# Kernel optimization log

Hardware: AMD Instinct MI355X
Metric: run time of the kernel (lower is better)

## Reference

```python
import jax, jax.numpy as jnp
import numpy as np

B, T, N, P, L = 8, 96, 20000, 12, 3
D = 32          # d_model (forced by channel-count identity d_model+96 == 4*d_model)
C = 4 * D       # 128 channels inside the linearized conv layers
M = 64          # random_feature_dim
TAU = 0.25
EPS = 1e-6      # numerical_stabilizer in random_feature_map


def _proj_matrix(m, d, seed=0):
    # create_random_matrix: stacked transposed-Q blocks from QR of gaussian blocks,
    # scaled row-wise by norms of a gaussian matrix (scaling=0).
    rng = np.random.RandomState(seed)
    blocks = []
    n_full = m // d
    for _ in range(n_full):
        q, _ = np.linalg.qr(rng.randn(d, d))
        blocks.append(q.T)
    rem = m - n_full * d
    if rem:
        q, _ = np.linalg.qr(rng.randn(d, d))
        blocks.append(q.T[:rem])
    mat = np.vstack(blocks)
    mult = np.linalg.norm(rng.randn(m, d), axis=1)
    return jnp.asarray(mult[:, None] * mat, dtype=jnp.float32)


def setup_inputs() -> dict:
    key = jax.random.key(0)
    ks = jax.random.split(key, 12)
    g = lambda k, shape, s=0.05: jax.random.normal(k, shape, jnp.float32) * s
    return {
        "x": jax.random.normal(ks[0], (B, T, N), jnp.float32),
        "x_mark": jax.random.uniform(ks[1], (B, T, 2), dtype=jnp.float32),
        "node_emb": g(ks[2], (N, D), 0.1),
        "time_tab": g(ks[3], (T, D), 0.1),
        "week_tab": g(ks[4], (7, D), 0.1),
        "input_w": g(ks[5], (D, 3 * T)),
        "input_b": jnp.zeros((D,), jnp.float32),
        "w1_w": g(ks[6], (D, 3 * D)),
        "w1_b": jnp.zeros((D,), jnp.float32),
        "w2_w": g(ks[7], (D, 3 * D)),
        "w2_b": jnp.zeros((D,), jnp.float32),
        "in_w": g(ks[8], (L, C, C)),
        "in_b": jnp.zeros((L, C), jnp.float32),
        "out_w": g(ks[9], (L, C, C)),
        "out_b": jnp.zeros((L, C), jnp.float32),
        "ln_g": jnp.ones((L, C), jnp.float32),
        "ln_b": jnp.zeros((L, C), jnp.float32),
        "reg_w": g(ks[10], (P, 2 * C)),
        "reg_b": jnp.zeros((P,), jnp.float32),
        "proj": _proj_matrix(M, D, seed=0),
    }


def _rfm(data, proj, is_query):
    # FAVOR+ positive random features (head dim == 1 folded out; shapes are [B,N,d])
    d = data.shape[-1]
    data = data * (float(d) ** -0.25)            # h(x) normalizer d^{-1/4}
    ratio = 1.0 / np.sqrt(float(proj.shape[0]))
    dash = jnp.einsum('bnd,md->bnm', data, proj)
    diag = 0.5 * jnp.sum(data * data, axis=-1, keepdims=True)
    if is_query:
        stab = jnp.max(dash, axis=-1, keepdims=True)          # per-row max
    else:
        stab = jnp.max(dash, axis=(1, 2), keepdims=True)      # max over features AND nodes
    return ratio * (jnp.exp(dash - diag - stab) + EPS)


def _linear_kernel(v, phi_q, phi_k):
    # associativity trick: (phi_q (phi_k^T v)) / (phi_q (phi_k^T 1))
    kv = jnp.einsum('bnm,bnc->bmc', phi_k, v)
    num = jnp.einsum('bnm,bmc->bnc', phi_q, kv)
    den = jnp.einsum('bnm,bm->bn', phi_q, jnp.sum(phi_k, axis=1))
    return num / den[..., None]


def reference(x, x_mark, node_emb, time_tab, week_tab, input_w, input_b,
              w1_w, w1_b, w2_w, w2_b, in_w, in_b, out_w, out_b,
              ln_g, ln_b, reg_w, reg_b, proj):
    Bq, Tq, Nq = x.shape
    marks = jax.lax.stop_gradient(x_mark)
    tod_idx = jnp.clip((marks[:, -1, 0] * Tq).astype(jnp.int32), 0, Tq - 1)
    dow_idx = jnp.clip((marks[:, -1, 1] * 7.0).astype(jnp.int32), 0, 6)
    time_e = jnp.broadcast_to(time_tab[tod_idx][:, None, :], (Bq, Nq, D))
    week_e = jnp.broadcast_to(week_tab[dow_idx][:, None, :], (Bq, Nq, D))
    node_e = jnp.broadcast_to(node_emb[None], (Bq, Nq, D))

    # input embedding over the flattened (feature-major) [3*T] channel axis
    tod_f = jnp.broadcast_to(x_mark[:, :, 0:1], (Bq, Tq, Nq))
    dow_f = jnp.broadcast_to(x_mark[:, :, 1:2], (Bq, Tq, Nq))
    feat = jnp.concatenate([x, tod_f, dow_f], axis=1)          # (B, 3T, N)
    x_in = jnp.einsum('bkn,ck->bnc', feat, input_w) + input_b  # (B, N, D)

    xg = jnp.concatenate([node_e, time_e, week_e], axis=-1)        # (B,N,3D)
    h = jnp.concatenate([x_in, node_e, time_e, week_e], axis=-1)   # (B,N,4D)

    inv_sqrt_tau = 1.0 / np.sqrt(TAU)
    nv1 = (jnp.einsum('bng,cg->bnc', xg, w1_w) + w1_b) * inv_sqrt_tau
    nv2 = (jnp.einsum('bng,cg->bnc', xg, w2_w) + w2_b) * inv_sqrt_tau
    # same node vectors (hence same data-derived seed / projection) every layer
    phi_q = _rfm(nv1, proj, True)    # (B,N,M)
    phi_k = _rfm(nv2, proj, False)   # (B,N,M)

    skip = h
    for i in range(L):
        res = h
        u = jax.nn.sigmoid(h @ in_w[i].T + in_b[i]) * (h @ out_w[i].T + out_b[i])
        u = _linear_kernel(u, phi_q, phi_k)
        h = u + res
        mu = jnp.mean(h, axis=-1, keepdims=True)
        var = jnp.var(h, axis=-1, keepdims=True)
        h = (h - mu) * jax.lax.rsqrt(var + 1e-5) * ln_g[i] + ln_b[i]

    out = jnp.concatenate([skip, h], axis=-1) @ reg_w.T + reg_b  # (B,N,P)
    return jnp.swapaxes(out, 1, 2)                               # (B,P,N)
```

## Files before the change

kernel.cpp:

```cpp
#include <hip/hip_runtime.h>

typedef unsigned short u16;
typedef __attribute__((ext_vector_type(8))) __bf16 bf16x8;
typedef __attribute__((ext_vector_type(4))) float f32x4;

#define BB 8
#define TT 96
#define NN 20000
#define NP 20160
#define PP 12
#define LL 3
#define DD 32
#define CC 128
#define MM 64
#define NB3 105
#define NB5 313
#define NB1 313

constexpr float KSC  = 0.8408964152537145f;
constexpr float KSC2 = 0.7071067811865476f;

__device__ inline u16 f2bf(float f){
  unsigned u = __float_as_uint(f);
  u = (u + 0x7fffu + ((u >> 16) & 1u)) >> 16;
  return (u16)u;
}
__device__ inline float bf2f(u16 h){ return __uint_as_float(((unsigned)h) << 16); }
__device__ inline unsigned fmapu(float f){
  unsigned u = __float_as_uint(f);
  return (u & 0x80000000u) ? ~u : (u | 0x80000000u);
}
__device__ inline float funmap(unsigned u){
  return (u & 0x80000000u) ? __uint_as_float(u & 0x7fffffffu) : __uint_as_float(~u);
}
__device__ inline unsigned pk2(float a, float b){
  return (unsigned)f2bf(a) | ((unsigned)f2bf(b) << 16);
}

__global__ void k0_prep(const float* xm, const float* time_tab, const float* week_tab,
                        const float* w1w, const float* w1b, const float* w2w, const float* w2b,
                        const float* inw, const float* inb, const float* proj,
                        float* bv1, float* bv2, float* sbd1, float* sbd2,
                        float* bc1, float* bc2, float* mb, int* tod, int* dow,
                        unsigned* cmx, float* ksum, float* qmat, float* emat)
{
  __shared__ float sT[BB][DD], sWk[BB][DD];
  __shared__ float sB1[BB][DD], sB2[BB][DD];
  __shared__ float sW1G[DD][DD], sW2G[DD][DD], sPJ[MM][DD];
  __shared__ int sTod[BB], sDow[BB];
  int tid = threadIdx.x;
  ksum[tid] = 0.f;
  for (int i = tid; i < DD*DD; i += 512){
    int c = i >> 5, g = i & 31;
    sW1G[c][g] = w1w[c*96 + g];
    sW2G[c][g] = w2w[c*96 + g];
  }
  for (int i = tid; i < MM*DD; i += 512) sPJ[i >> 5][i & 31] = proj[i];
  if (tid < BB){
    float t0 = xm[(tid*TT + TT-1)*2 + 0];
    float t1 = xm[(tid*TT + TT-1)*2 + 1];
    int ti = (int)(t0 * (float)TT); ti = min(max(ti, 0), TT-1);
    int di = (int)(t1 * 7.0f);      di = min(max(di, 0), 6);
    sTod[tid] = ti; sDow[tid] = di; tod[tid] = ti; dow[tid] = di;
  }
  if (tid < MM) cmx[tid] = fmapu(-3e38f);
  __syncthreads();
  if (tid < BB*DD){
    int b = tid >> 5, g = tid & 31;
    sT[b][g]  = time_tab[sTod[b]*DD + g];
    sWk[b][g] = week_tab[sDow[b]*DD + g];
  }
  __syncthreads();
  {
    int which = tid >> 8, b = (tid >> 5) & 7, c = tid & 31;
    const float* w  = which ? w2w : w1w;
    const float* wb = which ? w2b : w1b;
    float s = wb[c];
    for (int g = 0; g < DD; g++)
      s += sT[b][g]*w[c*96 + 32 + g] + sWk[b][g]*w[c*96 + 64 + g];
    if (which){ bv2[b*DD+c] = s; sB2[b][c] = s; }
    else      { bv1[b*DD+c] = s; sB1[b][c] = s; }
  }
  __syncthreads();
  for (int e = tid; e < 2*DD*MM; e += 512){
    int set = e >> 11, g = (e >> 6) & 31, m = e & 63;
    float s = 0.f;
    if (set == 0){ for (int c = 0; c < DD; c++) s += sW1G[c][g]*sPJ[m][c]; }
    else         { for (int c = 0; c < DD; c++) s += sW2G[c][g]*sPJ[m][c]; }
    qmat[e] = KSC * s;
  }
  {
    int set = tid >> 8, g = (tid >> 3) & 31, b = tid & 7;
    float s = 0.f;
    if (set == 0){ for (int c = 0; c < DD; c++) s += sW1G[c][g]*sB1[b][c]; }
    else         { for (int c = 0; c < DD; c++) s += sW2G[c][g]*sB2[b][c]; }
    emat[tid] = KSC2 * s;
  }
  {
    int b = tid >> 6, m = tid & 63;
    float s1 = 0.f, s2 = 0.f;
    for (int c = 0; c < DD; c++){
      float p = sPJ[m][c];
      s1 += sB1[b][c]*p; s2 += sB2[b][c]*p;
    }
    sbd1[b*MM+m] = KSC * s1;
    sbd2[b*MM+m] = KSC * s2;
  }
  if (tid < 16){
    int b = tid & 7;
    float s = 0.f;
    if (tid >> 3){ for (int c = 0; c < DD; c++) s += sB2[b][c]*sB2[b][c]; bc2[b] = 0.5f*KSC2*s; }
    else         { for (int c = 0; c < DD; c++) s += sB1[b][c]*sB1[b][c]; bc1[b] = 0.5f*KSC2*s; }
  }
  if (tid < 256){
    int b = tid >> 5, c = tid & 31;
    float s = inb[c];
    for (int t = 0; t < TT; t++){
      float m0 = xm[(b*TT+t)*2+0], m1 = xm[(b*TT+t)*2+1];
      s += m0 * inw[c*288 + 96 + t] + m1 * inw[c*288 + 192 + t];
    }
    mb[b*DD+c] = s;
  }
}

__global__ __launch_bounds__(256) void k1_node(
    const float* node_emb, const float* w1w, const float* w2w,
    const float* qmat, const float* emat,
    const float* gin_w, const float* gout_w,
    float* sd1, float* sd2, float* sq1, float* sq2,
    float* cr1, float* cr2, unsigned* cmx,
    u16* wbf, float* kvz)
{
  __shared__ float sQ1[DD*MM], sQ2[DD*MM];
  __shared__ float sW1[DD*DD], sW2[DD*DD];
  __shared__ float sE[2*DD*BB];
  __shared__ unsigned sCM[MM];
  int tid = threadIdx.x;
  int gid = blockIdx.x*256 + tid;
  const int TOT = NB1*256;
  for (int i = gid; i < LL*BB*MM*CC; i += TOT) kvz[i] = 0.f;
  for (int i = gid; i < 2*LL*CC*CC; i += TOT){
    int which = i / (LL*CC*CC);
    int r = i - which*(LL*CC*CC);
    wbf[i] = f2bf((which ? gout_w : gin_w)[r]);
  }
  for (int i = tid; i < DD*MM; i += 256){ sQ1[i] = qmat[i]; sQ2[i] = qmat[DD*MM + i]; }
  for (int i = tid; i < DD*DD; i += 256){
    sW1[i] = w1w[(i>>5)*96 + (i&31)];
    sW2[i] = w2w[(i>>5)*96 + (i&31)];
  }
  for (int i = tid; i < 2*DD*BB; i += 256) sE[i] = emat[i];
  if (tid < MM) sCM[tid] = fmapu(-3e38f);
  __syncthreads();
  int r = tid >> 2, q = tid & 3;
  int n = blockIdx.x*64 + r;
  bool valid = n < NN;
  int nc = valid ? n : 0;
  float nd[DD];
  #pragma unroll
  for (int g = 0; g < DD; g += 4){
    float4 v = *(const float4*)&node_emb[nc*DD + g];
    nd[g] = v.x; nd[g+1] = v.y; nd[g+2] = v.z; nd[g+3] = v.w;
  }
  float s1v[16], s2v[16];
  #pragma unroll
  for (int j = 0; j < 16; j++){ s1v[j] = 0.f; s2v[j] = 0.f; }
  #pragma unroll
  for (int g = 0; g < DD; g++){
    float xg = nd[g];
    #pragma unroll
    for (int jj = 0; jj < 16; jj += 4){
      float4 a1 = *(const float4*)&sQ1[g*MM + q*16 + jj];
      float4 a2 = *(const float4*)&sQ2[g*MM + q*16 + jj];
      s1v[jj+0] += xg*a1.x; s1v[jj+1] += xg*a1.y; s1v[jj+2] += xg*a1.z; s1v[jj+3] += xg*a1.w;
      s2v[jj+0] += xg*a2.x; s2v[jj+1] += xg*a2.y; s2v[jj+2] += xg*a2.z; s2v[jj+3] += xg*a2.w;
    }
  }
  if (valid){
    #pragma unroll
    for (int jj = 0; jj < 16; jj += 4){
      *(float4*)&sd1[(size_t)n*MM + q*16 + jj] = make_float4(s1v[jj], s1v[jj+1], s1v[jj+2], s1v[jj+3]);
      *(float4*)&sd2[(size_t)n*MM + q*16 + jj] = make_float4(s2v[jj], s2v[jj+1], s2v[jj+2], s2v[jj+3]);
    }
    #pragma unroll
    for (int j = 0; j < 16; j++)
      atomicMax(&sCM[q*16 + j], fmapu(s2v[j]));
  }
  float sqp1 = 0.f, sqp2 = 0.f;
  #pragma unroll
  for (int c8 = 0; c8 < 8; c8++){
    int c = q*8 + c8;
    float d1 = 0.f, d2 = 0.f;
    #pragma unroll
    for (int g = 0; g < DD; g += 4){
      float4 w1v = *(const float4*)&sW1[c*DD + g];
      float4 w2v = *(const float4*)&sW2[c*DD + g];
      d1 += nd[g]*w1v.x + nd[g+1]*w1v.y + nd[g+2]*w1v.z + nd[g+3]*w1v.w;
      d2 += nd[g]*w2v.x + nd[g+1]*w2v.y + nd[g+2]*w2v.z + nd[g+3]*w2v.w;
    }
    sqp1 += d1*d1; sqp2 += d2*d2;
  }
  sqp1 += __shfl_xor(sqp1, 1); sqp1 += __shfl_xor(sqp1, 2);
  sqp2 += __shfl_xor(sqp2, 1); sqp2 += __shfl_xor(sqp2, 2);
  if (q == 0 && valid){
    sq1[n] = 0.5f*KSC2*sqp1;
    sq2[n] = 0.5f*KSC2*sqp2;
  }
  {
    float cA1 = 0.f, cB1 = 0.f, cA2 = 0.f, cB2 = 0.f;
    #pragma unroll
    for (int g = 0; g < DD; g++){
      float xg = nd[g];
      cA1 += xg*sE[g*8 + 2*q];
      cB1 += xg*sE[g*8 + 2*q + 1];
      cA2 += xg*sE[256 + g*8 + 2*q];
      cB2 += xg*sE[256 + g*8 + 2*q + 1];
    }
    if (valid){
      cr1[(2*q)*NN + n]     = cA1;
      cr1[(2*q+1)*NN + n]   = cB1;
      cr2[(2*q)*NN + n]     = cA2;
      cr2[(2*q+1)*NN + n]   = cB2;
    }
  }
  __syncthreads();
  if (tid < MM) atomicMax(&cmx[tid], sCM[tid]);
}

__global__ void k0b_stab(const unsigned* cmx, const float* sbd2, float* stab){
  int lane = threadIdx.x;
  float cm = funmap(cmx[lane]);
  for (int b = 0; b < BB; b++){
    float v = cm + sbd2[b*MM + lane];
    #pragma unroll
    for (int off = 32; off; off >>= 1) v = fmaxf(v, __shfl_xor(v, off));
    if (lane == 0) stab[b] = v;
  }
}

__global__ __launch_bounds__(256) void k1b_phi(
    const float* sd1, const float* sd2, const float* sq1, const float* sq2,
    const float* cr1, const float* cr2, const float* sbd1, const float* sbd2,
    const float* bc1, const float* bc2, const float* stab,
    u16* phiq, u16* phikt, float* ksum)
{
  __shared__ u16 sT[MM][264];
  __shared__ float sQb[MM], sKb[MM];
  __shared__ float sRed[256];
  int tid = threadIdx.x;
  int b = blockIdx.y, n0 = blockIdx.x*256;
  if (tid < MM){
    sQb[tid] = sbd1[b*MM + tid];
    sKb[tid] = sbd2[b*MM + tid] - bc2[b] - stab[b];
  }
  __syncthreads();
  int n = n0 + tid;
  bool v = n < NN;
  int nc = v ? n : 0;
  float dq[MM];
  const float* s1r = sd1 + (size_t)nc*MM;
  #pragma unroll
  for (int m = 0; m < MM; m += 4){
    float4 t = *(const float4*)&s1r[m];
    dq[m]=t.x; dq[m+1]=t.y; dq[m+2]=t.z; dq[m+3]=t.w;
  }
  float rm = -3e38f;
  #pragma unroll
  for (int m = 0; m < MM; m++) rm = fmaxf(rm, dq[m] + sQb[m]);
  float diagq = sq1[nc] + cr1[b*NN + nc] + bc1[b];
  u16* pqr = phiq + ((size_t)(b*NN) + nc)*MM;
  #pragma unroll
  for (int m = 0; m < MM; m += 8){
    float p[8];
    #pragma unroll
    for (int j = 0; j < 8; j++){
      float ev = dq[m+j] + sQb[m+j] - rm - diagq;
      p[j] = 0.125f*__expf(ev) + 1.25e-7f;
    }
    uint4 w = { pk2(p[0],p[1]), pk2(p[2],p[3]), pk2(p[4],p[5]), pk2(p[6],p[7]) };
    if (v) *(uint4*)&pqr[m] = w;
  }
  const float* s2r = sd2 + (size_t)nc*MM;
  float diagk = sq2[nc] + cr2[b*NN + nc];
  #pragma unroll
  for (int m = 0; m < MM; m++){
    float ev = s2r[m] + sKb[m] - diagk;
    float pv = v ? (0.125f*__expf(ev) + 1.25e-7f) : 0.f;
    sT[m][tid] = f2bf(pv);
  }
  __syncthreads();
  {
    int m = tid >> 2, q = tid & 3;
    float s = 0.f;
    for (int j = 0; j < 64; j++) s += bf2f(sT[m][q*64 + j]);
    sRed[tid] = s;
  }
  __syncthreads();
  if (tid < MM){
    float s = sRed[tid*4] + sRed[tid*4+1] + sRed[tid*4+2] + sRed[tid*4+3];
    atomicAdd(&ksum[b*MM + tid], s);
  }
  {
    int m = tid >> 2, q = tid & 3;
    int nb = n0 + q*64;
    if (nb + 64 <= NP){
      u16* dst = phikt + (size_t)(b*MM + m)*NP + nb;
      #pragma unroll
      for (int j = 0; j < 64; j += 8)
        *(uint4*)&dst[j] = *(const uint4*)&sT[m][q*64 + j];
    }
  }
}

__global__ __launch_bounds__(256) void k2_embed(
    const float* x, const float* node_emb, const float* time_tab, const float* week_tab,
    const float* inw, const float* mb, const int* tod, const int* dow,
    u16* skip)
{
  __shared__ float sWt[TT*DD];
  __shared__ float sMB[DD], sTE[DD], sWE[DD];
  int tid = threadIdx.x;
  int b = blockIdx.y;
  for (int i = tid; i < TT*DD; i += 256){
    int t = i >> 5, c = i & 31;
    sWt[i] = inw[c*288 + t];
  }
  if (tid < DD){
    sMB[tid] = mb[b*DD + tid];
    sTE[tid] = time_tab[tod[b]*DD + tid];
    sWE[tid] = week_tab[dow[b]*DD + tid];
  }
  __syncthreads();
  int n = blockIdx.x*256 + tid;
  bool valid = n < NN;
  int nc = valid ? n : 0;
  float acc[DD];
  #pragma unroll
  for (int c = 0; c < DD; c++) acc[c] = sMB[c];
  const float* xb = x + (size_t)b*TT*NN + nc;
  for (int t = 0; t < TT; t++){
    float xv = xb[(size_t)t*NN];
    #pragma unroll
    for (int c = 0; c < DD; c++) acc[c] += xv * sWt[t*DD + c];
  }
  if (!valid) return;
  float nodev[DD];
  #pragma unroll
  for (int g = 0; g < DD; g += 4){
    float4 v = *(const float4*)&node_emb[n*DD + g];
    nodev[g] = v.x; nodev[g+1] = v.y; nodev[g+2] = v.z; nodev[g+3] = v.w;
  }
  auto chv = [&](int c)->float{
    if (c < 32)  return acc[c];
    if (c < 64)  return nodev[c-32];
    if (c < 96)  return sTE[c-64];
    return sWE[c-96];
  };
  u16* dst = skip + (size_t)(b*NN + n)*CC;
  #pragma unroll
  for (int g = 0; g < CC; g += 8){
    uint4 w;
    w.x = pk2(chv(g+0), chv(g+1));
    w.y = pk2(chv(g+2), chv(g+3));
    w.z = pk2(chv(g+4), chv(g+5));
    w.w = pk2(chv(g+6), chv(g+7));
    *(uint4*)&dst[g] = w;
  }
}

__global__ __launch_bounds__(256,2) void k3_gate(
    const u16* hin, const u16* wbf, const float* inb, const float* outb,
    const u16* phikt, float* kv, int layer)
{
  __shared__ u16 sUT[CC*72];
  __shared__ float s_inb[CC], s_outb[CC];
  int tid = threadIdx.x;
  int b = blockIdx.y, blk = blockIdx.x;
  int lane = tid & 63, wave = tid >> 6, quad = lane >> 4, l15 = lane & 15;
  if (tid < CC){ s_inb[tid] = inb[layer*CC + tid]; s_outb[tid] = outb[layer*CC + tid]; }

  bf16x8 bw[4][4];
  #pragma unroll
  for (int nt = 0; nt < 4; nt++){
    int which = nt >> 1;
    int co = wave*32 + (nt & 1)*16 + l15;
    const u16* wp = wbf + ((size_t)(which*LL + layer)*CC + co)*CC;
    #pragma unroll
    for (int ks = 0; ks < 4; ks++)
      bw[ks][nt] = *(const bf16x8*)&wp[ks*32 + quad*8];
  }
  f32x4 kvacc[4][2] = {};
  const u16* hbase = hin + (size_t)(b*NN)*CC;

  for (int ch = 0; ch < 3; ch++){
    int n0 = blk*192 + ch*64;
    f32x4 acc[4][4] = {};
    bf16x8 af[2][4];
    #pragma unroll
    for (int mt = 0; mt < 4; mt++)
      af[0][mt] = *(const bf16x8*)&hbase[(size_t)(n0 + mt*16 + l15)*CC + quad*8];
    #pragma unroll
    for (int ks = 0; ks < 4; ks++){
      int cur = ks & 1, nxt = cur ^ 1;
      if (ks < 3){
        #pragma unroll
        for (int mt = 0; mt < 4; mt++)
          af[nxt][mt] = *(const bf16x8*)&hbase[(size_t)(n0 + mt*16 + l15)*CC + (ks+1)*32 + quad*8];
      }
      #pragma unroll
      for (int mt = 0; mt < 4; mt++)
        #pragma unroll
        for (int nt = 0; nt < 4; nt++)
          acc[mt][nt] = __builtin_amdgcn_mfma_f32_16x16x32_bf16(af[cur][mt], bw[ks][nt], acc[mt][nt], 0, 0, 0);
    }
    __syncthreads();
    #pragma unroll
    for (int mt = 0; mt < 4; mt++){
      int r0 = mt*16 + quad*4;
      #pragma unroll
      for (int nt = 0; nt < 2; nt++){
        int co = wave*32 + nt*16 + l15;
        float bi = s_inb[co], bo = s_outb[co];
        float uv[4];
        #pragma unroll
        for (int e = 0; e < 4; e++){
          float up = acc[mt][nt][e] + bi;
          float vp = acc[mt][nt+2][e] + bo;
          float u = vp / (1.f + __expf(-up));
          if (n0 + r0 + e >= NN) u = 0.f;
          uv[e] = u;
        }
        ushort4 hv4;
        hv4.x = f2bf(uv[0]); hv4.y = f2bf(uv[1]); hv4.z = f2bf(uv[2]); hv4.w = f2bf(uv[3]);
        *(ushort4*)&sUT[co*72 + r0] = hv4;
      }
    }
    __syncthreads();
    #pragma unroll
    for (int ks2 = 0; ks2 < 2; ks2++){
      bf16x8 ap[4], bu[2];
      #pragma unroll
      for (int mtp = 0; mtp < 4; mtp++)
        ap[mtp] = *(const bf16x8*)&phikt[(size_t)(b*MM + mtp*16 + l15)*NP + n0 + ks2*32 + quad*8];
      #pragma unroll
      for (int nt2 = 0; nt2 < 2; nt2++)
        bu[nt2] = *(const bf16x8*)&sUT[(wave*32 + nt2*16 + l15)*72 + ks2*32 + quad*8];
      #pragma unroll
      for (int mtp = 0; mtp < 4; mtp++)
        #pragma unroll
        for (int nt2 = 0; nt2 < 2; nt2++)
          kvacc[mtp][nt2] = __builtin_amdgcn_mfma_f32_16x16x32_bf16(ap[mtp], bu[nt2], kvacc[mtp][nt2], 0, 0, 0);
    }
  }
  float* kvb = kv + (size_t)(layer*BB + b)*MM*CC;
  #pragma unroll
  for (int mt = 0; mt < 4; mt++)
    #pragma unroll
    for (int nt2 = 0; nt2 < 2; nt2++)
      #pragma unroll
      for (int e = 0; e < 4; e++)
        atomicAdd(&kvb[(mt*16 + quad*4 + e)*CC + wave*32 + nt2*16 + l15], kvacc[mt][nt2][e]);
}

__global__ void k4_reduce(const float* kv, const float* ksum, u16* kvt, int layer){
  int b = blockIdx.x;
  int tid = threadIdx.x;
  const float* kvb = kv + (size_t)(layer*BB + b)*MM*CC;
  for (int idx = tid; idx < 144*MM; idx += 256){
    int c = idx >> 6, m = idx & 63;
    float v = (c < CC) ? kvb[m*CC + c] : ((c == CC) ? ksum[b*MM + m] : 0.f);
    kvt[(size_t)b*144*MM + idx] = f2bf(v);
  }
}

__global__ __launch_bounds__(256) void k5_attn(
    const u16* hin, u16* hout, const u16* phiq, const u16* kvt,
    const float* lng, const float* lnb, int layer)
{
  __shared__ u16 sH[64*132];
  __shared__ u16 sKv[144*72];
  __shared__ float sLg[CC], sLb[CC];
  int tid = threadIdx.x;
  int b = blockIdx.y, n0 = blockIdx.x*64;
  int lane = tid & 63, wave = tid >> 6, quad = lane >> 4, l15 = lane & 15;
  for (int idx = tid; idx < 144*8; idx += 256){
    int c = idx >> 3, g = idx & 7;
    *(uint4*)&sKv[c*72 + g*8] = *(const uint4*)&kvt[(size_t)b*144*MM + c*MM + g*8];
  }
  if (tid < CC){ sLg[tid] = lng[layer*CC + tid]; sLb[tid] = lnb[layer*CC + tid]; }
  {
    int r = tid >> 2, seg = tid & 3;
    int n = n0 + r;
    const u16* src = hin + (size_t)(b*NN + min(n, NN-1))*CC + seg*32;
    #pragma unroll
    for (int k = 0; k < 32; k += 8){
      uint4 d = *(const uint4*)&src[k];
      *(uint2*)&sH[r*132 + seg*32 + k]     = make_uint2(d.x, d.y);
      *(uint2*)&sH[r*132 + seg*32 + k + 4] = make_uint2(d.z, d.w);
    }
  }
  __syncthreads();
  bf16x8 aq[2];
  #pragma unroll
  for (int ks = 0; ks < 2; ks++)
    aq[ks] = *(const bf16x8*)&phiq[((size_t)(b*NN) + n0 + wave*16 + l15)*MM + ks*32 + quad*8];
  f32x4 nacc[9] = {};
  #pragma unroll
  for (int ks = 0; ks < 2; ks++)
    #pragma unroll
    for (int nt = 0; nt < 9; nt++){
      bf16x8 bk = *(const bf16x8*)&sKv[(nt*16 + l15)*72 + ks*32 + quad*8];
      nacc[nt] = __builtin_amdgcn_mfma_f32_16x16x32_bf16(aq[ks], bk, nacc[nt], 0, 0, 0);
    }
  #pragma unroll
  for (int e = 0; e < 4; e++){
    float den = __shfl(nacc[8][e], lane & 48);
    int rml = wave*16 + quad*4 + e;
    float y[8];
    float s1 = 0.f, s2 = 0.f;
    #pragma unroll
    for (int nt = 0; nt < 8; nt++){
      float res = bf2f(sH[rml*132 + nt*16 + l15]);
      float yv = nacc[nt][e]/den + res;
      y[nt] = yv; s1 += yv; s2 += yv*yv;
    }
    #pragma unroll
    for (int off = 1; off < 16; off <<= 1){
      s1 += __shfl_xor(s1, off);
      s2 += __shfl_xor(s2, off);
    }
    float mu = s1 * (1.f/CC);
    float rs = rsqrtf(s2 * (1.f/CC) - mu*mu + 1e-5f);
    #pragma unroll
    for (int nt = 0; nt < 8; nt++){
      int c = nt*16 + l15;
      sH[rml*132 + c] = f2bf((y[nt] - mu)*rs*sLg[c] + sLb[c]);
    }
  }
  __syncthreads();
  {
    int r = tid >> 2, seg = tid & 3;
    int n = n0 + r;
    if (n < NN){
      u16* dst = hout + (size_t)(b*NN + n)*CC + seg*32;
      #pragma unroll
      for (int k = 0; k < 32; k += 8){
        uint2 a = *(const uint2*)&sH[r*132 + seg*32 + k];
        uint2 c2 = *(const uint2*)&sH[r*132 + seg*32 + k + 4];
        uint4 w = { a.x, a.y, c2.x, c2.y };
        *(uint4*)&dst[k] = w;
      }
    }
  }
}

__global__ __launch_bounds__(256) void k6_final(
    const u16* skip, const u16* hbuf, const float* regw, const float* regb,
    float* out)
{
  __shared__ float sRW[PP*256];
  __shared__ float sRB[PP];
  int tid = threadIdx.x;
  for (int i = tid; i < PP*256; i += 256) sRW[i] = regw[i];
  if (tid < PP) sRB[tid] = regb[tid];
  __syncthreads();
  int b = blockIdx.y;
  int n = blockIdx.x*256 + tid;
  if (n >= NN) return;
  float acc[PP];
  #pragma unroll
  for (int p = 0; p < PP; p++) acc[p] = sRB[p];
  const u16* sr = skip + (size_t)(b*NN + n)*CC;
  const u16* hr = hbuf + (size_t)(b*NN + n)*CC;
  for (int half = 0; half < 2; half++){
    const u16* src = half ? hr : sr;
    int coff = half*128;
    for (int k = 0; k < CC; k += 8){
      uint4 d = *(const uint4*)&src[k];
      float v0 = __uint_as_float(d.x<<16), v1 = __uint_as_float(d.x & 0xffff0000u);
      float v2 = __uint_as_float(d.y<<16), v3 = __uint_as_float(d.y & 0xffff0000u);
      float v4 = __uint_as_float(d.z<<16), v5 = __uint_as_float(d.z & 0xffff0000u);
      float v6 = __uint_as_float(d.w<<16), v7 = __uint_as_float(d.w & 0xffff0000u);
      #pragma unroll
      for (int p = 0; p < PP; p++){
        const float* wr = &sRW[p*256 + coff + k];
        acc[p] += v0*wr[0] + v1*wr[1] + v2*wr[2] + v3*wr[3]
                + v4*wr[4] + v5*wr[5] + v6*wr[6] + v7*wr[7];
      }
    }
  }
  #pragma unroll
  for (int p = 0; p < PP; p++)
    out[(size_t)(b*PP + p)*NN + n] = acc[p];
}

extern "C" void kernel_launch(void* const* d_in, const int* in_sizes, int n_in,
                              void* d_out, int out_size, void* d_ws, size_t ws_size,
                              hipStream_t stream)
{
  const float* x        = (const float*)d_in[0];
  const float* xm       = (const float*)d_in[1];
  const float* node_emb = (const float*)d_in[2];
  const float* time_tab = (const float*)d_in[3];
  const float* week_tab = (const float*)d_in[4];
  const float* input_w  = (const float*)d_in[5];
  const float* input_b  = (const float*)d_in[6];
  const float* w1w      = (const float*)d_in[7];
  const float* w1b      = (const float*)d_in[8];
  const float* w2w      = (const float*)d_in[9];
  const float* w2b      = (const float*)d_in[10];
  const float* inw      = (const float*)d_in[11];
  const float* inb      = (const float*)d_in[12];
  const float* outw     = (const float*)d_in[13];
  const float* outb     = (const float*)d_in[14];
  const float* lng      = (const float*)d_in[15];
  const float* lnb      = (const float*)d_in[16];
  const float* regw     = (const float*)d_in[17];
  const float* regb     = (const float*)d_in[18];
  const float* proj     = (const float*)d_in[19];
  float* out = (float*)d_out;

  char* wsb = (char*)d_ws;
  size_t off = 0;
  auto alloc = [&](size_t bytes)->char*{
    char* p = wsb + off; off += (bytes + 255) & ~(size_t)255; return p;
  };
  u16*   skip  = (u16*)  alloc((size_t)BB*NN*CC*2);
  u16*   hbuf  = (u16*)  alloc((size_t)BB*NN*CC*2);
  u16*   phiq  = (u16*)  alloc((size_t)BB*NN*MM*2);
  u16*   phikt = (u16*)  alloc((size_t)BB*MM*NP*2 + 4096);
  float* sd1   = (float*)alloc((size_t)NN*MM*4);
  float* sd2   = (float*)alloc((size_t)NN*MM*4);
  float* sq1   = (float*)alloc((size_t)NN*4);
  float* sq2   = (float*)alloc((size_t)NN*4);
  float* cr1   = (float*)alloc((size_t)BB*NN*4);
  float* cr2   = (float*)alloc((size_t)BB*NN*4);
  u16*   wbf   = (u16*)  alloc((size_t)2*LL*CC*CC*2);
  float* kv    = (float*)alloc((size_t)LL*BB*MM*CC*4);
  u16*   kvt   = (u16*)  alloc((size_t)BB*144*MM*2);
  float* ksum  = (float*)alloc(BB*MM*4);
  float* bv1   = (float*)alloc(BB*DD*4);
  float* bv2   = (float*)alloc(BB*DD*4);
  float* sbd1  = (float*)alloc(BB*MM*4);
  float* sbd2  = (float*)alloc(BB*MM*4);
  float* bc1   = (float*)alloc(BB*4);
  float* bc2   = (float*)alloc(BB*4);
  float* mb    = (float*)alloc(BB*DD*4);
  int*   tod   = (int*)  alloc(BB*4);
  int*   dow   = (int*)  alloc(BB*4);
  unsigned* cmx= (unsigned*)alloc(MM*4);
  float* stab  = (float*)alloc(BB*4);
  float* qmat  = (float*)alloc(2*DD*MM*4);
  float* emat  = (float*)alloc(2*DD*BB*4);
  (void)ws_size; (void)in_sizes; (void)n_in; (void)out_size;

  k0_prep<<<1, 512, 0, stream>>>(xm, time_tab, week_tab, w1w, w1b, w2w, w2b,
                                 input_w, input_b, proj,
                                 bv1, bv2, sbd1, sbd2, bc1, bc2, mb, tod, dow, cmx, ksum,
                                 qmat, emat);
  k1_node<<<NB1, 256, 0, stream>>>(node_emb, w1w, w2w, qmat, emat, inw, outw,
                                   sd1, sd2, sq1, sq2, cr1, cr2, cmx, wbf, kv);
  k0b_stab<<<1, 64, 0, stream>>>(cmx, sbd2, stab);
  k1b_phi<<<dim3(79, 8), 256, 0, stream>>>(sd1, sd2, sq1, sq2, cr1, cr2,
                                           sbd1, sbd2, bc1, bc2, stab,
                                           phiq, phikt, ksum);
  k2_embed<<<dim3(79, 8), 256, 0, stream>>>(x, node_emb, time_tab, week_tab,
                                            input_w, mb, tod, dow, skip);
  for (int l = 0; l < LL; l++){
    const u16* hi = (l == 0) ? skip : hbuf;
    k3_gate<<<dim3(NB3, 8), 256, 0, stream>>>(hi, wbf, inb, outb, phikt, kv, l);
    k4_reduce<<<8, 256, 0, stream>>>(kv, ksum, kvt, l);
    k5_attn<<<dim3(NB5, 8), 256, 0, stream>>>(hi, hbuf, phiq, kvt, lng, lnb, l);
  }
  k6_final<<<dim3(79, 8), 256, 0, stream>>>(skip, hbuf, regw, regb, out);
}
```

Baseline: 661.1 us.

## Make gate and attention kernels wave-private to drop block barriers

In the gate kernel, each wave now gets its own shared-memory slice for the transposed gated activations, and the biases are loaded into registers, so the two __syncthreads per chunk go away. In the attention kernel, the KV matrix is read straight from global memory rather than staged in LDS, and the LayerNorm gamma/beta move into registers. Each wave now owns the 16 rows it loads and writes back, so both block barriers are removed. This trades barrier and LDS staging cost for more global/cache reads of the KV matrix per wave and more register use.

```diff
diff --git a/kernel.cpp b/kernel.cpp
--- a/kernel.cpp
+++ b/kernel.cpp
@@ -372,13 +372,19 @@
     const u16* hin, const u16* wbf, const float* inb, const float* outb,
     const u16* phikt, float* kv, int layer)
 {
-  __shared__ u16 sUT[CC*72];
-  __shared__ float s_inb[CC], s_outb[CC];
+  __shared__ u16 sUT[4][32*72];
   int tid = threadIdx.x;
   int b = blockIdx.y, blk = blockIdx.x;
   int lane = tid & 63, wave = tid >> 6, quad = lane >> 4, l15 = lane & 15;
-  if (tid < CC){ s_inb[tid] = inb[layer*CC + tid]; s_outb[tid] = outb[layer*CC + tid]; }
-
+  u16* myUT = &sUT[wave][0];
+
+  float bi[2], bo[2];
+  #pragma unroll
+  for (int nt = 0; nt < 2; nt++){
+    int co = wave*32 + nt*16 + l15;
+    bi[nt] = inb[layer*CC + co];
+    bo[nt] = outb[layer*CC + co];
+  }
   bf16x8 bw[4][4];
   #pragma unroll
   for (int nt = 0; nt < 4; nt++){
@@ -413,29 +419,26 @@
         for (int nt = 0; nt < 4; nt++)
           acc[mt][nt] = __builtin_amdgcn_mfma_f32_16x16x32_bf16(af[cur][mt], bw[ks][nt], acc[mt][nt], 0, 0, 0);
     }
-    __syncthreads();
     #pragma unroll
     for (int mt = 0; mt < 4; mt++){
       int r0 = mt*16 + quad*4;
       #pragma unroll
       for (int nt = 0; nt < 2; nt++){
-        int co = wave*32 + nt*16 + l15;
-        float bi = s_inb[co], bo = s_outb[co];
+        int cop = nt*16 + l15;
         float uv[4];
         #pragma unroll
         for (int e = 0; e < 4; e++){
-          float up = acc[mt][nt][e] + bi;
-          float vp = acc[mt][nt+2][e] + bo;
+          float up = acc[mt][nt][e] + bi[nt];
+          float vp = acc[mt][nt+2][e] + bo[nt];
           float u = vp / (1.f + __expf(-up));
           if (n0 + r0 + e >= NN) u = 0.f;
           uv[e] = u;
         }
         ushort4 hv4;
         hv4.x = f2bf(uv[0]); hv4.y = f2bf(uv[1]); hv4.z = f2bf(uv[2]); hv4.w = f2bf(uv[3]);
-        *(ushort4*)&sUT[co*72 + r0] = hv4;
+        *(ushort4*)&myUT[cop*72 + r0] = hv4;
       }
     }
-    __syncthreads();
     #pragma unroll
     for (int ks2 = 0; ks2 < 2; ks2++){
       bf16x8 ap[4], bu[2];
@@ -444,7 +447,7 @@
         ap[mtp] = *(const bf16x8*)&phikt[(size_t)(b*MM + mtp*16 + l15)*NP + n0 + ks2*32 + quad*8];
       #pragma unroll
       for (int nt2 = 0; nt2 < 2; nt2++)
-        bu[nt2] = *(const bf16x8*)&sUT[(wave*32 + nt2*16 + l15)*72 + ks2*32 + quad*8];
+        bu[nt2] = *(const bf16x8*)&myUT[(nt2*16 + l15)*72 + ks2*32 + quad*8];
       #pragma unroll
       for (int mtp = 0; mtp < 4; mtp++)
         #pragma unroll
@@ -478,18 +481,12 @@
     const float* lng, const float* lnb, int layer)
 {
   __shared__ u16 sH[64*132];
-  __shared__ u16 sKv[144*72];
-  __shared__ float sLg[CC], sLb[CC];
   int tid = threadIdx.x;
   int b = blockIdx.y, n0 = blockIdx.x*64;
   int lane = tid & 63, wave = tid >> 6, quad = lane >> 4, l15 = lane & 15;
-  for (int idx = tid; idx < 144*8; idx += 256){
-    int c = idx >> 3, g = idx & 7;
-    *(uint4*)&sKv[c*72 + g*8] = *(const uint4*)&kvt[(size_t)b*144*MM + c*MM + g*8];
-  }
-  if (tid < CC){ sLg[tid] = lng[layer*CC + tid]; sLb[tid] = lnb[layer*CC + tid]; }
-  {
-    int r = tid >> 2, seg = tid & 3;
+  const u16* kvb = kvt + (size_t)b*144*MM;
+  {
+    int r = wave*16 + (lane >> 2), seg = lane & 3;
     int n = n0 + r;
     const u16* src = hin + (size_t)(b*NN + min(n, NN-1))*CC + seg*32;
     #pragma unroll
@@ -499,7 +496,6 @@
       *(uint2*)&sH[r*132 + seg*32 + k + 4] = make_uint2(d.z, d.w);
     }
   }
-  __syncthreads();
   bf16x8 aq[2];
   #pragma unroll
   for (int ks = 0; ks < 2; ks++)
@@ -509,9 +505,15 @@
   for (int ks = 0; ks < 2; ks++)
     #pragma unroll
     for (int nt = 0; nt < 9; nt++){
-      bf16x8 bk = *(const bf16x8*)&sKv[(nt*16 + l15)*72 + ks*32 + quad*8];
+      bf16x8 bk = *(const bf16x8*)&kvb[(nt*16 + l15)*MM + ks*32 + quad*8];
       nacc[nt] = __builtin_amdgcn_mfma_f32_16x16x32_bf16(aq[ks], bk, nacc[nt], 0, 0, 0);
     }
+  float lg[8], lb[8];
+  #pragma unroll
+  for (int nt = 0; nt < 8; nt++){
+    lg[nt] = lng[layer*CC + nt*16 + l15];
+    lb[nt] = lnb[layer*CC + nt*16 + l15];
+  }
   #pragma unroll
   for (int e = 0; e < 4; e++){
     float den = __shfl(nacc[8][e], lane & 48);
@@ -534,12 +536,11 @@
     #pragma unroll
     for (int nt = 0; nt < 8; nt++){
       int c = nt*16 + l15;
-      sH[rml*132 + c] = f2bf((y[nt] - mu)*rs*sLg[c] + sLb[c]);
-    }
-  }
-  __syncthreads();
-  {
-    int r = tid >> 2, seg = tid & 3;
+      sH[rml*132 + c] = f2bf((y[nt] - mu)*rs*lg[nt] + lb[nt]);
+    }
+  }
+  {
+    int r = wave*16 + (lane >> 2), seg = lane & 3;
     int n = n0 + r;
     if (n < NN){
       u16* dst = hout + (size_t)(b*NN + n)*CC + seg*32;
```

Measured after the change: 661.9 us. Within noise of the previous version (+0.1%).
